# Kernel tuning notes

Measured on AMD Instinct MI355X. Metric: run time of the kernel, lower is better.

The kernel has to match this reference:

```python
import jax, jax.numpy as jnp
import numpy as np

SR = 16000
NYQ = SR / 2.0
N_FFT = 400
HOP = 160
WIN = 400
OUT_CHANNELS = 64
OUTPUT_SIZE = 64
MIN_LOW_HZ = 50.0
MIN_BAND_HZ = 50.0
FRAME_LENGTH = 400
EPS_LN = 1e-5


def _to_mel(hz):
    return 2595.0 * np.log10(1.0 + hz / 700.0)


def _to_hz(mel):
    return 700.0 * (10.0 ** (mel / 2595.0) - 1.0)


def setup_inputs() -> dict:
    key = jax.random.key(0)
    k1, = jax.random.split(key, 1)
    waveforms = jax.random.normal(k1, (1024, 1, 16000), dtype=jnp.float32)
    # mel-spaced init, exactly as in __init__ (freq_init='mel', range_constraint=False)
    low_hz = 30.0
    high_hz = NYQ - (MIN_LOW_HZ + MIN_BAND_HZ)
    mel = np.linspace(_to_mel(low_hz), _to_mel(high_hz), OUT_CHANNELS + 1)
    hz = _to_hz(mel)
    low_hz_ = jnp.asarray(hz[:-1], dtype=jnp.float32).reshape(-1, 1)
    band_hz_ = jnp.asarray(np.diff(hz), dtype=jnp.float32).reshape(-1, 1)
    ln_weight = jnp.ones((OUT_CHANNELS, 1), dtype=jnp.float32)
    ln_bias = jnp.zeros((OUT_CHANNELS, 1), dtype=jnp.float32)
    return {
        "waveforms": waveforms,
        "low_hz_": low_hz_,
        "band_hz_": band_hz_,
        "ln_weight": ln_weight,
        "ln_bias": ln_bias,
    }


def _hann_periodic(n):
    # torch.hann_window default: periodic=True
    k = jnp.arange(n, dtype=jnp.float32)
    return 0.5 - 0.5 * jnp.cos(2.0 * jnp.pi * k / n)


def _stft_mag(x):
    pad = N_FFT // 2
    xp = jnp.pad(x, ((0, 0), (pad, pad)), mode="reflect")
    n_frames = 1 + (xp.shape[1] - N_FFT) // HOP
    idx = jnp.arange(n_frames)[:, None] * HOP + jnp.arange(N_FFT)[None, :]
    frames = xp[:, idx] * _hann_periodic(WIN)  # [B, F_t, n_fft]
    spec = jnp.fft.rfft(frames, axis=-1)       # [B, F_t, n_fft//2+1]
    return jnp.abs(spec).transpose(0, 2, 1)    # [B, n_fft//2+1, F_t]


def _get_filters(low_hz_, band_hz_):
    # vectorized over all channels (original loops per channel)
    low = MIN_LOW_HZ + jnp.abs(low_hz_)                                   # [C,1]
    high = jnp.clip(low + MIN_BAND_HZ + jnp.abs(band_hz_), MIN_LOW_HZ, NYQ)
    freq = jnp.linspace(0.0, NYQ, N_FFT // 2 + 1, dtype=jnp.float32)      # [F]
    mask = (freq >= low) & (freq <= high)                                 # [C,F]
    center = (low + high) / 2.0
    bw = high - low
    resp = 1.0 - jnp.abs(freq - center) / (bw / 2.0)                      # triangular
    return jnp.where(mask, resp, 0.0)                                     # [C,F]


def _gln(x, weight, bias):
    # GlobalLayerNorm over dims (1,2) of [B,C,T]
    mean = jnp.mean(x, axis=(1, 2), keepdims=True)
    var = jnp.mean((x - mean) ** 2, axis=(1, 2), keepdims=True)
    return weight * (x - mean) / jnp.sqrt(var + EPS_LN) + bias


def _interp_linear(x, out_size):
    # torch F.interpolate(mode='linear', align_corners=False) along last dim
    t_in = x.shape[-1]
    scale = t_in / out_size
    pos = (jnp.arange(out_size, dtype=jnp.float32) + 0.5) * scale - 0.5
    pos = jnp.clip(pos, 0.0, t_in - 1)
    i0 = jnp.floor(pos).astype(jnp.int32)
    i1 = jnp.minimum(i0 + 1, t_in - 1)
    w = (pos - i0.astype(jnp.float32))
    return x[..., i0] * (1.0 - w) + x[..., i1] * w


def reference(waveforms, low_hz_, band_hz_, ln_weight, ln_bias):
    B = waveforms.shape[0]
    target_length = HOP * (OUTPUT_SIZE - 1) + FRAME_LENGTH  # 10480
    cur = waveforms.shape[-1]
    x = waveforms[:, 0, :]
    if target_length > cur:  # static shape decision
        x = jnp.pad(x, ((0, 0), (0, target_length - cur)))
    mag_spec = _stft_mag(x)                       # [B, 201, F_t]
    filters = _get_filters(low_hz_, band_hz_)     # [C, 201]
    filtered = jnp.einsum("cf,bft->bct", filters, mag_spec)  # [B, C, F_t]
    filtered = _gln(filtered, ln_weight, ln_bias)
    energy = filtered ** 2
    log_energy = jnp.log10(energy + 1e-6)         # [B, C, F_t]
    if log_energy.shape[-1] != OUTPUT_SIZE:
        log_energy = _interp_linear(log_energy, OUTPUT_SIZE)  # [B, C, 64]
    log_energy = log_energy[:, None, :, :].transpose(0, 1, 3, 2)  # [B,1,64,C]
    return (log_energy, filters)
```

## Files before the change

kernel.cpp:

```cpp
#include <hip/hip_runtime.h>
#include <math.h>

typedef __attribute__((ext_vector_type(8))) short short8;
typedef __attribute__((ext_vector_type(16))) float f32x16;
typedef __attribute__((ext_vector_type(8))) float f32x8;

__device__ inline unsigned short f2bf(float x) {
    unsigned u = __float_as_uint(x);
    unsigned r = u + 0x7fffu + ((u >> 16) & 1u);
    return (unsigned short)(r >> 16);
}

struct ASplit { short8 h, l; };

__device__ inline ASplit splitA(f32x8 v) {
    unsigned ah[4], al[4];
    #pragma unroll
    for (int q = 0; q < 4; ++q) {
        unsigned short h0 = f2bf(v[2*q]),   h1 = f2bf(v[2*q+1]);
        float hf0 = __uint_as_float((unsigned)h0 << 16);
        float hf1 = __uint_as_float((unsigned)h1 << 16);
        unsigned short l0 = f2bf(v[2*q] - hf0), l1 = f2bf(v[2*q+1] - hf1);
        ah[q] = (unsigned)h0 | ((unsigned)h1 << 16);
        al[q] = (unsigned)l0 | ((unsigned)l1 << 16);
    }
    ASplit r;
    r.h = __builtin_bit_cast(short8, *(uint4*)ah);
    r.l = __builtin_bit_cast(short8, *(uint4*)al);
    return r;
}

__device__ inline f32x8 loadA8(const float* __restrict__ x, int i0) {
    f32x8 r;
    if (i0 >= 0 && i0 <= 15992) {
        float4 a0 = *(const float4*)(x + i0);
        float4 a1 = *(const float4*)(x + i0 + 4);
        r[0] = a0.x; r[1] = a0.y; r[2] = a0.z; r[3] = a0.w;
        r[4] = a1.x; r[5] = a1.y; r[6] = a1.z; r[7] = a1.w;
    } else {
        #pragma unroll
        for (int e = 0; e < 8; ++e) {
            int p = i0 + e;
            p = (p < 0) ? -p : p;
            p = (p > 15999) ? (31998 - p) : p;
            r[e] = x[p];
        }
    }
    return r;
}

__device__ inline void filter_params(int c, const float* low_hz_, const float* band_hz_,
                                     float* fctr, float* finv, int* fks, int* fke) {
    float lo = 50.0f + fabsf(low_hz_[c]);
    float hi = lo + 50.0f + fabsf(band_hz_[c]);
    hi = fminf(fmaxf(hi, 50.0f), 8000.0f);
    float ctr = 0.5f * (lo + hi);
    float hbw = 0.5f * (hi - lo);
    int ks = (int)ceilf(lo * 0.025f);
    if (ks < 0) ks = 0;
    while (40.0f * (float)ks < lo) ++ks;
    while (ks > 0 && 40.0f * (float)(ks - 1) >= lo) --ks;
    int ke = (int)floorf(hi * 0.025f);
    if (ke > 200) ke = 200;
    while (40.0f * (float)ke > hi) --ke;
    while (ke < 200 && 40.0f * (float)(ke + 1) <= hi) ++ke;
    fctr[c] = ctr;
    finv[c] = (hbw > 0.0f) ? (1.0f / hbw) : 0.0f;
    fks[c]  = ks;
    fke[c]  = ke;
}

__global__ void fse_filters(const float* __restrict__ low_hz_,
                            const float* __restrict__ band_hz_,
                            float* __restrict__ out)
{
    int idx = blockIdx.x * 256 + threadIdx.x;
    if (idx >= 64 * 201) return;
    int c = idx / 201;
    int k = idx - c * 201;
    float lo = 50.0f + fabsf(low_hz_[c]);
    float hi = lo + 50.0f + fabsf(band_hz_[c]);
    hi = fminf(fmaxf(hi, 50.0f), 8000.0f);
    float ctr = 0.5f * (lo + hi);
    float hbw = 0.5f * (hi - lo);
    float fq = 40.0f * (float)k;
    float resp = 1.0f - fabsf(fq - ctr) / hbw;
    out[idx] = (fq >= lo && fq <= hi) ? resp : 0.0f;
}

__global__ void fse_setup_B(unsigned short* __restrict__ bt)
{
    int idx = blockIdx.x * 256 + threadIdx.x;
    if (idx >= 372736) return;
    int e   = idx & 7;
    int t   = idx >> 3;
    int row = t % 448;
    int q   = t / 448;
    int p   = q & 3;
    int pl  = (q >> 2) & 1;
    int kc  = q >> 3;
    int n   = kc * 32 + p * 8 + e;
    float v = 0.0f;
    if (n < 400) {
        int bin = -1, isim = 0;
        if (row <= 200) bin = row;
        else if (row >= 224 && row <= 424) { bin = row - 224; isim = 1; }
        if (bin >= 0) {
            int a = (bin * n) % 400;
            float th = 6.283185307179586f * ((float)a / 400.0f);
            float sn, cs;
            sincosf(th, &sn, &cs);
            float wn = 0.5f - 0.5f * cosf(6.283185307179586f * ((float)n / 400.0f));
            v = isim ? (-wn * sn) : (wn * cs);
        }
    }
    unsigned short h = f2bf(v);
    float hf = __uint_as_float((unsigned)h << 16);
    unsigned short l = f2bf(v - hf);
    bt[idx] = pl ? l : h;
}

__global__ __launch_bounds__(512, 4)
void fse_gemm(const float* __restrict__ wav,
              const float* __restrict__ low_hz_,
              const float* __restrict__ band_hz_,
              const unsigned short* __restrict__ Bt,
              float* __restrict__ filt)
{
    __shared__ __align__(16) char smem[57344];
    __shared__ float fctr[64], finv[64];
    __shared__ int   fks[64], fke[64];
    float* mags = (float*)smem;

    const int bid  = blockIdx.x;
    const int b    = bid >> 1;
    const int half = bid & 1;
    const int tid  = threadIdx.x;
    const int w    = tid >> 6;
    const int lane = tid & 63;
    const float* __restrict__ x = wav + b * 16000;

    if (tid < 64) filter_params(tid, low_hz_, band_hz_, fctr, finv, fks, fke);

    const int mt    = w >> 2;
    const int pq    = w & 3;
    const int pbase = pq * 2;
    const int cnt   = (pq < 3) ? 2 : 1;
    const int jrow  = lane & 31;
    const int g     = lane >> 5;

    const int arow = 64 * half + 32 * mt + jrow;
    const int te   = (arow <= 100) ? arow : 50;
    const int ab   = 160 * te - 200 + g * 8;

    f32x16 accR[2], accI[2];
    #pragma unroll
    for (int i = 0; i < 2; ++i)
        #pragma unroll
        for (int e = 0; e < 16; ++e) { accR[i][e] = 0.0f; accI[i][e] = 0.0f; }

    for (int kc = 0; kc < 13; ++kc) {
        __syncthreads();
        {
            const uint4* src = (const uint4*)Bt + kc * 3584 + (w << 6) + lane;
            char* dstb = smem + (w << 6) * 16;
            #pragma unroll
            for (int i = 0; i < 7; ++i) {
                __builtin_amdgcn_global_load_lds(
                    (const __attribute__((address_space(1))) unsigned*)(src + i * 512),
                    (__attribute__((address_space(3))) unsigned*)(dstb + i * 8192),
                    16, 0, 0);
            }
        }
        __syncthreads();

        f32x8 a0 = loadA8(x, ab + kc * 32);
        f32x8 a1 = loadA8(x, ab + kc * 32 + 16);

        const unsigned short* bs = (const unsigned short*)smem;
        #pragma unroll
        for (int s = 0; s < 2; ++s) {
            ASplit S = splitA(s ? a1 : a0);
            const int part = s * 2 + g;
            const int bhof = part * 3584;
            const int blof = (4 + part) * 3584;
            #pragma unroll
            for (int i = 0; i < 2; ++i) {
                if (i < cnt) {
                    const int p = pbase + i;
                    const int roR = p * 32 + jrow;
                    const int roI = (p + 7) * 32 + jrow;
                    short8 BhR = *(const short8*)(bs + bhof + roR * 8);
                    short8 BlR = *(const short8*)(bs + blof + roR * 8);
                    short8 BhI = *(const short8*)(bs + bhof + roI * 8);
                    short8 BlI = *(const short8*)(bs + blof + roI * 8);
                    accR[i] = __builtin_amdgcn_mfma_f32_32x32x16_bf16(S.h, BhR, accR[i], 0, 0, 0);
                    accR[i] = __builtin_amdgcn_mfma_f32_32x32x16_bf16(S.h, BlR, accR[i], 0, 0, 0);
                    accR[i] = __builtin_amdgcn_mfma_f32_32x32x16_bf16(S.l, BhR, accR[i], 0, 0, 0);
                    accI[i] = __builtin_amdgcn_mfma_f32_32x32x16_bf16(S.h, BhI, accI[i], 0, 0, 0);
                    accI[i] = __builtin_amdgcn_mfma_f32_32x32x16_bf16(S.h, BlI, accI[i], 0, 0, 0);
                    accI[i] = __builtin_amdgcn_mfma_f32_32x32x16_bf16(S.l, BhI, accI[i], 0, 0, 0);
                }
            }
        }
    }

    __syncthreads();

    #pragma unroll
    for (int i = 0; i < 2; ++i) {
        if (i < cnt) {
            const int k = (pbase + i) * 32 + jrow;
            if (k <= 200) {
                #pragma unroll
                for (int r = 0; r < 16; ++r) {
                    int tl = 32 * mt + (r & 3) + 8 * (r >> 2) + 4 * g;
                    float re = accR[i][r];
                    float im = accI[i][r];
                    mags[tl * 201 + k] = sqrtf(re * re + im * im);
                }
            }
        }
    }
    __syncthreads();

    const int tg = 64 * half + lane;
    #pragma unroll
    for (int i = 0; i < 8; ++i) {
        const int c = w * 8 + i;
        const float ctr = fctr[c];
        const float inv = finv[c];
        const int ks = fks[c], ke = fke[c];
        float a = 0.0f;
        for (int k = ks; k <= ke; ++k) {
            float resp = 1.0f - fabsf(40.0f * (float)k - ctr) * inv;
            a = fmaf(resp, mags[lane * 201 + k], a);
        }
        if (tg <= 100) filt[b * 6464 + c * 101 + tg] = a;
    }
}

__global__ __launch_bounds__(256)
void fse_post(const float* __restrict__ filt,
              const float* __restrict__ ln_w,
              const float* __restrict__ ln_b,
              float* __restrict__ out)
{
    __shared__ float fbuf[6464];
    __shared__ float red[8];
    __shared__ float stats[2];
    const int b    = blockIdx.x;
    const int tid  = threadIdx.x;
    const int w    = tid >> 6;
    const int lane = tid & 63;
    const float* __restrict__ src = filt + b * 6464;

    float s = 0.0f, ss = 0.0f;
    for (int i = tid; i < 6464; i += 256) {
        float v = src[i];
        fbuf[i] = v;
        s += v;
        ss = fmaf(v, v, ss);
    }
    #pragma unroll
    for (int off = 32; off > 0; off >>= 1) {
        s  += __shfl_down(s,  off, 64);
        ss += __shfl_down(ss, off, 64);
    }
    if (lane == 0) { red[w] = s; red[4 + w] = ss; }
    __syncthreads();
    if (tid == 0) {
        float ts = 0.0f, tss = 0.0f;
        for (int i = 0; i < 4; ++i) { ts += red[i]; tss += red[4 + i]; }
        float mu = ts * (1.0f / 6464.0f);
        stats[0] = mu;
        stats[1] = tss * (1.0f / 6464.0f) - mu * mu;
    }
    __syncthreads();
    const float mu   = stats[0];
    const float isig = 1.0f / sqrtf(stats[1] + 1e-5f);

    for (int idx = tid; idx < 4096; idx += 256) {
        const int to = idx >> 6;
        const int c  = idx & 63;
        float pos = ((float)to + 0.5f) * 1.578125f - 0.5f;
        pos = fminf(fmaxf(pos, 0.0f), 100.0f);
        int i0 = (int)floorf(pos);
        int i1 = i0 + 1; if (i1 > 100) i1 = 100;
        float fr = pos - (float)i0;
        float wc = ln_w[c], bc = ln_b[c];
        float x0 = fbuf[c * 101 + i0];
        float x1 = fbuf[c * 101 + i1];
        float y0 = fmaf(wc, (x0 - mu) * isig, bc);
        float y1 = fmaf(wc, (x1 - mu) * isig, bc);
        float l0 = log10f(fmaf(y0, y0, 1e-6f));
        float l1 = log10f(fmaf(y1, y1, 1e-6f));
        out[b * 4096 + idx] = l0 * (1.0f - fr) + l1 * fr;
    }
}

#define MSTR 209
__global__ __launch_bounds__(512, 2)
void fse_main_fused(const float* __restrict__ wav,
                    const float* __restrict__ low_hz_,
                    const float* __restrict__ band_hz_,
                    const float* __restrict__ ln_w,
                    const float* __restrict__ ln_b,
                    const unsigned short* __restrict__ Bt,
                    float* __restrict__ out)
{
    __shared__ __align__(16) char smem[114688];
    float* mags = (float*)smem;
    float* fbuf = (float*)(smem + 84544);
    __shared__ float fctr[64], finv[64];
    __shared__ int   fks[64], fke[64];
    __shared__ float red[16];
    __shared__ float stats[2];

    const int b    = blockIdx.x;
    const int tid  = threadIdx.x;
    const int w    = tid >> 6;
    const int lane = tid & 63;
    const float* __restrict__ x = wav + b * 16000;

    if (tid < 64) filter_params(tid, low_hz_, band_hz_, fctr, finv, fks, fke);

    const int mt   = w >> 1;
    const int half = w & 1;
    const int jrow = lane & 31;
    const int g    = lane >> 5;
    const int arow = mt * 32 + jrow;
    const int te   = (arow <= 100) ? arow : 50;
    const int abase = 160 * te - 200 + g * 8;

    const uint4* __restrict__ btg = (const uint4*)Bt;

    f32x8 ac0 = loadA8(x, abase);
    f32x8 ac1 = loadA8(x, abase + 16);
    {
        uint4 rr0 = btg[0 * 512 + tid], rr1 = btg[1 * 512 + tid];
        uint4 rr2 = btg[2 * 512 + tid], rr3 = btg[3 * 512 + tid];
        uint4 rr4 = btg[4 * 512 + tid], rr5 = btg[5 * 512 + tid];
        uint4 rr6 = btg[6 * 512 + tid];
        uint4* dst = (uint4*)smem;
        dst[0 * 512 + tid] = rr0; dst[1 * 512 + tid] = rr1;
        dst[2 * 512 + tid] = rr2; dst[3 * 512 + tid] = rr3;
        dst[4 * 512 + tid] = rr4; dst[5 * 512 + tid] = rr5;
        dst[6 * 512 + tid] = rr6;
    }
    __syncthreads();

    f32x16 acc[7];
    #pragma unroll
    for (int n = 0; n < 7; ++n)
        #pragma unroll
        for (int e = 0; e < 16; ++e) acc[n][e] = 0.0f;

    int curoff = 0;
    for (int kc = 0; kc < 13; ++kc) {
        const bool pre = (kc < 12);
        uint4 rr0, rr1, rr2, rr3, rr4, rr5, rr6;
        f32x8 an0, an1;
        if (pre) {
            const uint4* src = btg + (kc + 1) * 3584;
            rr0 = src[0 * 512 + tid]; rr1 = src[1 * 512 + tid];
            rr2 = src[2 * 512 + tid]; rr3 = src[3 * 512 + tid];
            rr4 = src[4 * 512 + tid]; rr5 = src[5 * 512 + tid];
            rr6 = src[6 * 512 + tid];
            an0 = loadA8(x, abase + (kc + 1) * 32);
            an1 = loadA8(x, abase + (kc + 1) * 32 + 16);
        }
        ASplit A0 = splitA(ac0);
        ASplit A1 = splitA(ac1);

        const unsigned short* bs = (const unsigned short*)(smem + curoff);
        #pragma unroll
        for (int s = 0; s < 2; ++s) {
            const short8 Ah = s ? A1.h : A0.h;
            const short8 Al = s ? A1.l : A0.l;
            const int pb = (s * 2 + g) * 448;
            #pragma unroll
            for (int n = 0; n < 7; ++n) {
                const int ro = (half * 7 + n) * 32 + jrow;
                short8 Bh = *(const short8*)(bs + (pb + ro) * 8);
                short8 Bl = *(const short8*)(bs + 14336 + (pb + ro) * 8);
                acc[n] = __builtin_amdgcn_mfma_f32_32x32x16_bf16(Ah, Bh, acc[n], 0, 0, 0);
                acc[n] = __builtin_amdgcn_mfma_f32_32x32x16_bf16(Ah, Bl, acc[n], 0, 0, 0);
                acc[n] = __builtin_amdgcn_mfma_f32_32x32x16_bf16(Al, Bh, acc[n], 0, 0, 0);
            }
        }
        if (pre) {
            uint4* dst = (uint4*)(smem + (curoff ^ 57344));
            dst[0 * 512 + tid] = rr0; dst[1 * 512 + tid] = rr1;
            dst[2 * 512 + tid] = rr2; dst[3 * 512 + tid] = rr3;
            dst[4 * 512 + tid] = rr4; dst[5 * 512 + tid] = rr5;
            dst[6 * 512 + tid] = rr6;
        }
        __syncthreads();
        if (pre) { ac0 = an0; ac1 = an1; }
        curoff ^= 57344;
    }

    if (half == 0) {
        #pragma unroll
        for (int n = 0; n < 7; ++n) {
            int k = n * 32 + jrow;
            if (k <= 200) {
                #pragma unroll
                for (int r = 0; r < 16; ++r) {
                    int t = mt * 32 + (r & 3) + 8 * (r >> 2) + 4 * g;
                    if (t <= 100) mags[t * MSTR + k] = acc[n][r];
                }
            }
        }
    }
    __syncthreads();
    if (half == 1) {
        #pragma unroll
        for (int n = 0; n < 7; ++n) {
            int k = n * 32 + jrow;
            if (k <= 200) {
                #pragma unroll
                for (int r = 0; r < 16; ++r) {
                    int t = mt * 32 + (r & 3) + 8 * (r >> 2) + 4 * g;
                    if (t <= 100) {
                        float re = mags[t * MSTR + k];
                        float im = acc[n][r];
                        mags[t * MSTR + k] = sqrtf(re * re + im * im);
                    }
                }
            }
        }
    }
    __syncthreads();

    {
        const int t0 = lane;
        const int t1v = 64 + lane;
        const int t1 = (t1v <= 100) ? t1v : 100;
        #pragma unroll
        for (int i = 0; i < 8; ++i) {
            const int c = w * 8 + i;
            const float ctr = fctr[c];
            const float inv = finv[c];
            const int ks = fks[c], ke = fke[c];
            float a0 = 0.0f, a1 = 0.0f;
            for (int k = ks; k <= ke; ++k) {
                float resp = 1.0f - fabsf(40.0f * (float)k - ctr) * inv;
                a0 = fmaf(resp, mags[t0 * MSTR + k], a0);
                a1 = fmaf(resp, mags[t1 * MSTR + k], a1);
            }
            fbuf[c * 101 + t0] = a0;
            if (t1v <= 100) fbuf[c * 101 + t1v] = a1;
        }
    }
    __syncthreads();

    float s = 0.0f, ss = 0.0f;
    for (int i = tid; i < 6464; i += 512) {
        float vv = fbuf[i];
        s += vv;
        ss = fmaf(vv, vv, ss);
    }
    #pragma unroll
    for (int off = 32; off > 0; off >>= 1) {
        s  += __shfl_down(s,  off, 64);
        ss += __shfl_down(ss, off, 64);
    }
    if (lane == 0) { red[w] = s; red[8 + w] = ss; }
    __syncthreads();
    if (tid == 0) {
        float ts = 0.0f, tss = 0.0f;
        for (int i = 0; i < 8; ++i) { ts += red[i]; tss += red[8 + i]; }
        float mu = ts * (1.0f / 6464.0f);
        stats[0] = mu;
        stats[1] = tss * (1.0f / 6464.0f) - mu * mu;
    }
    __syncthreads();
    const float mu   = stats[0];
    const float isig = 1.0f / sqrtf(stats[1] + 1e-5f);

    for (int idx = tid; idx < 4096; idx += 512) {
        const int to = idx >> 6;
        const int c  = idx & 63;
        float pos = ((float)to + 0.5f) * 1.578125f - 0.5f;
        pos = fminf(fmaxf(pos, 0.0f), 100.0f);
        int i0 = (int)floorf(pos);
        int i1 = i0 + 1; if (i1 > 100) i1 = 100;
        float fr = pos - (float)i0;
        float wc = ln_w[c], bc = ln_b[c];
        float x0 = fbuf[c * 101 + i0];
        float x1 = fbuf[c * 101 + i1];
        float y0 = fmaf(wc, (x0 - mu) * isig, bc);
        float y1 = fmaf(wc, (x1 - mu) * isig, bc);
        float l0 = log10f(fmaf(y0, y0, 1e-6f));
        float l1 = log10f(fmaf(y1, y1, 1e-6f));
        out[b * 4096 + idx] = l0 * (1.0f - fr) + l1 * fr;
    }
}

extern "C" void kernel_launch(void* const* d_in, const int* in_sizes, int n_in,
                              void* d_out, int out_size, void* d_ws, size_t ws_size,
                              hipStream_t stream)
{
    const float* wav = (const float*)d_in[0];
    const float* lo  = (const float*)d_in[1];
    const float* bd  = (const float*)d_in[2];
    const float* lw  = (const float*)d_in[3];
    const float* lb  = (const float*)d_in[4];
    float* out = (float*)d_out;

    fse_filters<<<(64 * 201 + 255) / 256, 256, 0, stream>>>(lo, bd, out + 1024 * 4096);

    const size_t BN1 = 745472;
    const size_t BN2 = BN1 + (size_t)1024 * 6464 * 4;
    unsigned short* Bts = (unsigned short*)d_ws;
    fse_setup_B<<<(372736 + 255) / 256, 256, 0, stream>>>(Bts);

    if (ws_size >= BN2) {
        float* filt = (float*)((char*)d_ws + BN1);
        fse_gemm<<<2048, 512, 0, stream>>>(wav, lo, bd, Bts, filt);
        fse_post<<<1024, 256, 0, stream>>>(filt, lw, lb, out);
    } else {
        fse_main_fused<<<1024, 512, 0, stream>>>(wav, lo, bd, lw, lb, Bts, out);
    }
}
```

Measured before the change: 249.7 us.

## Double-buffer B tiles in LDS with prefetch and cheaper bf16 split

Result: faster. 222.8 us (-10.8%).

```diff
diff --git a/kernel.cpp b/kernel.cpp
--- a/kernel.cpp
+++ b/kernel.cpp
@@ -27,6 +27,23 @@
     ASplit r;
     r.h = __builtin_bit_cast(short8, *(uint4*)ah);
     r.l = __builtin_bit_cast(short8, *(uint4*)al);
+    return r;
+}
+
+__device__ inline ASplit splitA_fast(f32x8 v) {
+    unsigned h[4], l[4];
+    #pragma unroll
+    for (int q = 0; q < 4; ++q) {
+        unsigned u0 = __float_as_uint(v[2*q]);
+        unsigned u1 = __float_as_uint(v[2*q+1]);
+        h[q] = __builtin_amdgcn_perm(u1, u0, 0x07060302u);
+        float r0 = v[2*q]   - __uint_as_float(u0 & 0xFFFF0000u);
+        float r1 = v[2*q+1] - __uint_as_float(u1 & 0xFFFF0000u);
+        l[q] = __builtin_amdgcn_perm(__float_as_uint(r1), __float_as_uint(r0), 0x07060302u);
+    }
+    ASplit r;
+    r.h = __builtin_bit_cast(short8, *(uint4*)h);
+    r.l = __builtin_bit_cast(short8, *(uint4*)l);
     return r;
 }
 
@@ -88,7 +105,39 @@
     out[idx] = (fq >= lo && fq <= hi) ? resp : 0.0f;
 }
 
-__global__ void fse_setup_B(unsigned short* __restrict__ bt)
+__global__ void fse_setup_B16(unsigned short* __restrict__ bt)
+{
+    int idx = blockIdx.x * 256 + threadIdx.x;
+    if (idx >= 372736) return;
+    int e   = idx & 7;
+    int t   = idx >> 3;
+    int row = t % 448;
+    int q   = t / 448;
+    int g   = q & 1;
+    int pl  = (q >> 1) & 1;
+    int kc  = q >> 2;
+    int n   = kc * 16 + g * 8 + e;
+    float v = 0.0f;
+    if (n < 400) {
+        int bin = -1, isim = 0;
+        if (row <= 200) bin = row;
+        else if (row >= 224 && row <= 424) { bin = row - 224; isim = 1; }
+        if (bin >= 0) {
+            int a = (bin * n) % 400;
+            float th = 6.283185307179586f * ((float)a / 400.0f);
+            float sn, cs;
+            sincosf(th, &sn, &cs);
+            float wn = 0.5f - 0.5f * cosf(6.283185307179586f * ((float)n / 400.0f));
+            v = isim ? (-wn * sn) : (wn * cs);
+        }
+    }
+    unsigned short h = f2bf(v);
+    float hf = __uint_as_float((unsigned)h << 16);
+    unsigned short l = f2bf(v - hf);
+    bt[idx] = pl ? l : h;
+}
+
+__global__ void fse_setup_B32(unsigned short* __restrict__ bt)
 {
     int idx = blockIdx.x * 256 + threadIdx.x;
     if (idx >= 372736) return;
@@ -153,59 +202,75 @@
     const int te   = (arow <= 100) ? arow : 50;
     const int ab   = 160 * te - 200 + g * 8;
 
+    const uint4* __restrict__ btg = (const uint4*)Bt;
+
+    f32x8 aC = loadA8(x, ab);
+    {
+        #pragma unroll
+        for (int i = 0; i < 4; ++i) {
+            int idx = i * 512 + tid;
+            if (idx < 1792) {
+                __builtin_amdgcn_global_load_lds(
+                    (const __attribute__((address_space(1))) unsigned*)(btg + idx),
+                    (__attribute__((address_space(3))) unsigned*)(smem + idx * 16),
+                    16, 0, 0);
+            }
+        }
+    }
+    __syncthreads();
+
     f32x16 accR[2], accI[2];
     #pragma unroll
     for (int i = 0; i < 2; ++i)
         #pragma unroll
         for (int e = 0; e < 16; ++e) { accR[i][e] = 0.0f; accI[i][e] = 0.0f; }
 
-    for (int kc = 0; kc < 13; ++kc) {
+    int cur = 0;
+    for (int kc = 0; kc < 26; ++kc) {
+        const bool pre = (kc < 25);
+        f32x8 aN;
+        if (pre) {
+            const uint4* src = btg + (kc + 1) * 1792;
+            const int bufo = cur ^ 28672;
+            #pragma unroll
+            for (int i = 0; i < 4; ++i) {
+                int idx = i * 512 + tid;
+                if (idx < 1792) {
+                    __builtin_amdgcn_global_load_lds(
+                        (const __attribute__((address_space(1))) unsigned*)(src + idx),
+                        (__attribute__((address_space(3))) unsigned*)(smem + bufo + idx * 16),
+                        16, 0, 0);
+                }
+            }
+            aN = loadA8(x, ab + (kc + 1) * 16);
+        }
+
+        ASplit S = splitA_fast(aC);
+
+        const unsigned short* bs = (const unsigned short*)(smem + cur);
+        #pragma unroll
+        for (int i = 0; i < 2; ++i) {
+            if (i < cnt) {
+                const int p = pbase + i;
+                const int roR = p * 32 + jrow;
+                const int roI = (p + 7) * 32 + jrow;
+                short8 BhR = *(const short8*)(bs + ((0 + g) * 448 + roR) * 8);
+                short8 BlR = *(const short8*)(bs + ((2 + g) * 448 + roR) * 8);
+                short8 BhI = *(const short8*)(bs + ((0 + g) * 448 + roI) * 8);
+                short8 BlI = *(const short8*)(bs + ((2 + g) * 448 + roI) * 8);
+                accR[i] = __builtin_amdgcn_mfma_f32_32x32x16_bf16(S.h, BhR, accR[i], 0, 0, 0);
+                accR[i] = __builtin_amdgcn_mfma_f32_32x32x16_bf16(S.h, BlR, accR[i], 0, 0, 0);
+                accR[i] = __builtin_amdgcn_mfma_f32_32x32x16_bf16(S.l, BhR, accR[i], 0, 0, 0);
+                accI[i] = __builtin_amdgcn_mfma_f32_32x32x16_bf16(S.h, BhI, accI[i], 0, 0, 0);
+                accI[i] = __builtin_amdgcn_mfma_f32_32x32x16_bf16(S.h, BlI, accI[i], 0, 0, 0);
+                accI[i] = __builtin_amdgcn_mfma_f32_32x32x16_bf16(S.l, BhI, accI[i], 0, 0, 0);
+            }
+        }
+
         __syncthreads();
-        {
-            const uint4* src = (const uint4*)Bt + kc * 3584 + (w << 6) + lane;
-            char* dstb = smem + (w << 6) * 16;
-            #pragma unroll
-            for (int i = 0; i < 7; ++i) {
-                __builtin_amdgcn_global_load_lds(
-                    (const __attribute__((address_space(1))) unsigned*)(src + i * 512),
-                    (__attribute__((address_space(3))) unsigned*)(dstb + i * 8192),
-                    16, 0, 0);
-            }
-        }
-        __syncthreads();
-
-        f32x8 a0 = loadA8(x, ab + kc * 32);
-        f32x8 a1 = loadA8(x, ab + kc * 32 + 16);
-
-        const unsigned short* bs = (const unsigned short*)smem;
-        #pragma unroll
-        for (int s = 0; s < 2; ++s) {
-            ASplit S = splitA(s ? a1 : a0);
-            const int part = s * 2 + g;
-            const int bhof = part * 3584;
-            const int blof = (4 + part) * 3584;
-            #pragma unroll
-            for (int i = 0; i < 2; ++i) {
-                if (i < cnt) {
-                    const int p = pbase + i;
-                    const int roR = p * 32 + jrow;
-                    const int roI = (p + 7) * 32 + jrow;
-                    short8 BhR = *(const short8*)(bs + bhof + roR * 8);
-                    short8 BlR = *(const short8*)(bs + blof + roR * 8);
-                    short8 BhI = *(const short8*)(bs + bhof + roI * 8);
-                    short8 BlI = *(const short8*)(bs + blof + roI * 8);
-                    accR[i] = __builtin_amdgcn_mfma_f32_32x32x16_bf16(S.h, BhR, accR[i], 0, 0, 0);
-                    accR[i] = __builtin_amdgcn_mfma_f32_32x32x16_bf16(S.h, BlR, accR[i], 0, 0, 0);
-                    accR[i] = __builtin_amdgcn_mfma_f32_32x32x16_bf16(S.l, BhR, accR[i], 0, 0, 0);
-                    accI[i] = __builtin_amdgcn_mfma_f32_32x32x16_bf16(S.h, BhI, accI[i], 0, 0, 0);
-                    accI[i] = __builtin_amdgcn_mfma_f32_32x32x16_bf16(S.h, BlI, accI[i], 0, 0, 0);
-                    accI[i] = __builtin_amdgcn_mfma_f32_32x32x16_bf16(S.l, BhI, accI[i], 0, 0, 0);
-                }
-            }
-        }
-    }
-
-    __syncthreads();
+        if (pre) aC = aN;
+        cur ^= 28672;
+    }
 
     #pragma unroll
     for (int i = 0; i < 2; ++i) {
@@ -515,13 +580,14 @@
     const size_t BN1 = 745472;
     const size_t BN2 = BN1 + (size_t)1024 * 6464 * 4;
     unsigned short* Bts = (unsigned short*)d_ws;
-    fse_setup_B<<<(372736 + 255) / 256, 256, 0, stream>>>(Bts);
 
     if (ws_size >= BN2) {
         float* filt = (float*)((char*)d_ws + BN1);
+        fse_setup_B16<<<(372736 + 255) / 256, 256, 0, stream>>>(Bts);
         fse_gemm<<<2048, 512, 0, stream>>>(wav, lo, bd, Bts, filt);
         fse_post<<<1024, 256, 0, stream>>>(filt, lw, lb, out);
     } else {
+        fse_setup_B32<<<(372736 + 255) / 256, 256, 0, stream>>>(Bts);
         fse_main_fused<<<1024, 512, 0, stream>>>(wav, lo, bd, lw, lb, Bts, out);
     }
 }
```

## Fuse GEMM and post-processing into one 1024-thread kernel with double-buffered LDS

Applied to the files above, without the earlier changes.

After: 219.5 us. -12.1%, faster.

```diff
diff --git a/kernel.cpp b/kernel.cpp
--- a/kernel.cpp
+++ b/kernel.cpp
@@ -1,5 +1,8 @@
 #include <hip/hip_runtime.h>
 #include <math.h>
+
+#define BLOCK 1024
+#define MSTR 209
 
 typedef __attribute__((ext_vector_type(8))) short short8;
 typedef __attribute__((ext_vector_type(16))) float f32x16;
@@ -13,20 +16,20 @@
 
 struct ASplit { short8 h, l; };
 
-__device__ inline ASplit splitA(f32x8 v) {
-    unsigned ah[4], al[4];
+__device__ inline ASplit splitA_fast(f32x8 v) {
+    unsigned h[4], l[4];
     #pragma unroll
     for (int q = 0; q < 4; ++q) {
-        unsigned short h0 = f2bf(v[2*q]),   h1 = f2bf(v[2*q+1]);
-        float hf0 = __uint_as_float((unsigned)h0 << 16);
-        float hf1 = __uint_as_float((unsigned)h1 << 16);
-        unsigned short l0 = f2bf(v[2*q] - hf0), l1 = f2bf(v[2*q+1] - hf1);
-        ah[q] = (unsigned)h0 | ((unsigned)h1 << 16);
-        al[q] = (unsigned)l0 | ((unsigned)l1 << 16);
+        unsigned u0 = __float_as_uint(v[2*q]);
+        unsigned u1 = __float_as_uint(v[2*q+1]);
+        h[q] = __builtin_amdgcn_perm(u1, u0, 0x07060302u);
+        float r0 = v[2*q]   - __uint_as_float(u0 & 0xFFFF0000u);
+        float r1 = v[2*q+1] - __uint_as_float(u1 & 0xFFFF0000u);
+        l[q] = __builtin_amdgcn_perm(__float_as_uint(r1), __float_as_uint(r0), 0x07060302u);
     }
     ASplit r;
-    r.h = __builtin_bit_cast(short8, *(uint4*)ah);
-    r.l = __builtin_bit_cast(short8, *(uint4*)al);
+    r.h = __builtin_bit_cast(short8, *(uint4*)h);
+    r.l = __builtin_bit_cast(short8, *(uint4*)l);
     return r;
 }
 
@@ -120,21 +123,25 @@
     bt[idx] = pl ? l : h;
 }
 
-__global__ __launch_bounds__(512, 4)
-void fse_gemm(const float* __restrict__ wav,
+__global__ __launch_bounds__(1024, 4)
+void fse_main(const float* __restrict__ wav,
               const float* __restrict__ low_hz_,
               const float* __restrict__ band_hz_,
+              const float* __restrict__ ln_w,
+              const float* __restrict__ ln_b,
               const unsigned short* __restrict__ Bt,
-              float* __restrict__ filt)
+              float* __restrict__ out)
 {
-    __shared__ __align__(16) char smem[57344];
+    __shared__ __align__(16) char smem[114688];
+    float* mags = (float*)smem;
+    float* fbuf = (float*)(smem + 84544);
+
     __shared__ float fctr[64], finv[64];
     __shared__ int   fks[64], fke[64];
-    float* mags = (float*)smem;
-
-    const int bid  = blockIdx.x;
-    const int b    = bid >> 1;
-    const int half = bid & 1;
+    __shared__ float red[32];
+    __shared__ float stats[2];
+
+    const int b    = blockIdx.x;
     const int tid  = threadIdx.x;
     const int w    = tid >> 6;
     const int lane = tid & 63;
@@ -149,9 +156,27 @@
     const int jrow  = lane & 31;
     const int g     = lane >> 5;
 
-    const int arow = 64 * half + 32 * mt + jrow;
+    const int arow = 32 * mt + jrow;
     const int te   = (arow <= 100) ? arow : 50;
     const int ab   = 160 * te - 200 + g * 8;
+
+    const uint4* __restrict__ btg = (const uint4*)Bt;
+
+    f32x8 aC0 = loadA8(x, ab);
+    f32x8 aC1 = loadA8(x, ab + 16);
+    {
+        #pragma unroll
+        for (int i = 0; i < 4; ++i) {
+            int idx = i * 1024 + tid;
+            if (idx < 3584) {
+                __builtin_amdgcn_global_load_lds(
+                    (const __attribute__((address_space(1))) unsigned*)(btg + idx),
+                    (__attribute__((address_space(3))) unsigned*)(smem + idx * 16),
+                    16, 0, 0);
+            }
+        }
+    }
+    __syncthreads();
 
     f32x16 accR[2], accI[2];
     #pragma unroll
@@ -159,28 +184,35 @@
         #pragma unroll
         for (int e = 0; e < 16; ++e) { accR[i][e] = 0.0f; accI[i][e] = 0.0f; }
 
+    int cur = 0;
     for (int kc = 0; kc < 13; ++kc) {
-        __syncthreads();
-        {
-            const uint4* src = (const uint4*)Bt + kc * 3584 + (w << 6) + lane;
-            char* dstb = smem + (w << 6) * 16;
+        const bool pre = (kc < 12);
+
+        ASplit S0 = splitA_fast(aC0);
+        ASplit S1 = splitA_fast(aC1);
+
+        if (pre) {
+            const uint4* src = btg + (kc + 1) * 3584;
+            const int bufo = cur ^ 57344;
             #pragma unroll
-            for (int i = 0; i < 7; ++i) {
-                __builtin_amdgcn_global_load_lds(
-                    (const __attribute__((address_space(1))) unsigned*)(src + i * 512),
-                    (__attribute__((address_space(3))) unsigned*)(dstb + i * 8192),
-                    16, 0, 0);
-            }
-        }
-        __syncthreads();
-
-        f32x8 a0 = loadA8(x, ab + kc * 32);
-        f32x8 a1 = loadA8(x, ab + kc * 32 + 16);
-
-        const unsigned short* bs = (const unsigned short*)smem;
+            for (int i = 0; i < 4; ++i) {
+                int idx = i * 1024 + tid;
+                if (idx < 3584) {
+                    __builtin_amdgcn_global_load_lds(
+                        (const __attribute__((address_space(1))) unsigned*)(src + idx),
+                        (__attribute__((address_space(3))) unsigned*)(smem + bufo + idx * 16),
+                        16, 0, 0);
+                }
+            }
+            aC0 = loadA8(x, ab + (kc + 1) * 32);
+            aC1 = loadA8(x, ab + (kc + 1) * 32 + 16);
+        }
+
+        const unsigned short* bs = (const unsigned short*)(smem + cur);
         #pragma unroll
         for (int s = 0; s < 2; ++s) {
-            ASplit S = splitA(s ? a1 : a0);
+            const short8 Ah = s ? S1.h : S0.h;
+            const short8 Al = s ? S1.l : S0.l;
             const int part = s * 2 + g;
             const int bhof = part * 3584;
             const int blof = (4 + part) * 3584;
@@ -194,18 +226,19 @@
                     short8 BlR = *(const short8*)(bs + blof + roR * 8);
                     short8 BhI = *(const short8*)(bs + bhof + roI * 8);
                     short8 BlI = *(const short8*)(bs + blof + roI * 8);
-                    accR[i] = __builtin_amdgcn_mfma_f32_32x32x16_bf16(S.h, BhR, accR[i], 0, 0, 0);
-                    accR[i] = __builtin_amdgcn_mfma_f32_32x32x16_bf16(S.h, BlR, accR[i], 0, 0, 0);
-                    accR[i] = __builtin_amdgcn_mfma_f32_32x32x16_bf16(S.l, BhR, accR[i], 0, 0, 0);
-                    accI[i] = __builtin_amdgcn_mfma_f32_32x32x16_bf16(S.h, BhI, accI[i], 0, 0, 0);
-                    accI[i] = __builtin_amdgcn_mfma_f32_32x32x16_bf16(S.h, BlI, accI[i], 0, 0, 0);
-                    accI[i] = __builtin_amdgcn_mfma_f32_32x32x16_bf16(S.l, BhI, accI[i], 0, 0, 0);
+                    accR[i] = __builtin_amdgcn_mfma_f32_32x32x16_bf16(Ah, BhR, accR[i], 0, 0, 0);
+                    accR[i] = __builtin_amdgcn_mfma_f32_32x32x16_bf16(Ah, BlR, accR[i], 0, 0, 0);
+                    accR[i] = __builtin_amdgcn_mfma_f32_32x32x16_bf16(Al, BhR, accR[i], 0, 0, 0);
+                    accI[i] = __builtin_amdgcn_mfma_f32_32x32x16_bf16(Ah, BhI, accI[i], 0, 0, 0);
+                    accI[i] = __builtin_amdgcn_mfma_f32_32x32x16_bf16(Ah, BlI, accI[i], 0, 0, 0);
+                    accI[i] = __builtin_amdgcn_mfma_f32_32x32x16_bf16(Al, BhI, accI[i], 0, 0, 0);
                 }
             }
         }
-    }
-
-    __syncthreads();
+
+        __syncthreads();
+        cur ^= 57344;
+    }
 
     #pragma unroll
     for (int i = 0; i < 2; ++i) {
@@ -214,64 +247,56 @@
             if (k <= 200) {
                 #pragma unroll
                 for (int r = 0; r < 16; ++r) {
-                    int tl = 32 * mt + (r & 3) + 8 * (r >> 2) + 4 * g;
-                    float re = accR[i][r];
-                    float im = accI[i][r];
-                    mags[tl * 201 + k] = sqrtf(re * re + im * im);
+                    int t = 32 * mt + (r & 3) + 8 * (r >> 2) + 4 * g;
+                    if (t <= 100) {
+                        float re = accR[i][r];
+                        float im = accI[i][r];
+                        mags[t * MSTR + k] = sqrtf(re * re + im * im);
+                    }
                 }
             }
         }
     }
     __syncthreads();
 
-    const int tg = 64 * half + lane;
-    #pragma unroll
-    for (int i = 0; i < 8; ++i) {
-        const int c = w * 8 + i;
-        const float ctr = fctr[c];
-        const float inv = finv[c];
-        const int ks = fks[c], ke = fke[c];
-        float a = 0.0f;
-        for (int k = ks; k <= ke; ++k) {
-            float resp = 1.0f - fabsf(40.0f * (float)k - ctr) * inv;
-            a = fmaf(resp, mags[lane * 201 + k], a);
-        }
-        if (tg <= 100) filt[b * 6464 + c * 101 + tg] = a;
-    }
-}
-
-__global__ __launch_bounds__(256)
-void fse_post(const float* __restrict__ filt,
-              const float* __restrict__ ln_w,
-              const float* __restrict__ ln_b,
-              float* __restrict__ out)
-{
-    __shared__ float fbuf[6464];
-    __shared__ float red[8];
-    __shared__ float stats[2];
-    const int b    = blockIdx.x;
-    const int tid  = threadIdx.x;
-    const int w    = tid >> 6;
-    const int lane = tid & 63;
-    const float* __restrict__ src = filt + b * 6464;
+    {
+        const int t0 = lane;
+        const int t1v = 64 + lane;
+        const int t1 = (t1v <= 100) ? t1v : 100;
+        #pragma unroll
+        for (int i = 0; i < 4; ++i) {
+            const int c = w * 4 + i;
+            const float ctr = fctr[c];
+            const float inv = finv[c];
+            const int ks = fks[c], ke = fke[c];
+            float a0 = 0.0f, a1 = 0.0f;
+            for (int k = ks; k <= ke; ++k) {
+                float resp = 1.0f - fabsf(40.0f * (float)k - ctr) * inv;
+                a0 = fmaf(resp, mags[t0 * MSTR + k], a0);
+                a1 = fmaf(resp, mags[t1 * MSTR + k], a1);
+            }
+            fbuf[c * 101 + t0] = a0;
+            if (t1v <= 100) fbuf[c * 101 + t1v] = a1;
+        }
+    }
+    __syncthreads();
 
     float s = 0.0f, ss = 0.0f;
-    for (int i = tid; i < 6464; i += 256) {
-        float v = src[i];
-        fbuf[i] = v;
-        s += v;
-        ss = fmaf(v, v, ss);
+    for (int i = tid; i < 6464; i += BLOCK) {
+        float vv = fbuf[i];
+        s += vv;
+        ss = fmaf(vv, vv, ss);
     }
     #pragma unroll
     for (int off = 32; off > 0; off >>= 1) {
         s  += __shfl_down(s,  off, 64);
         ss += __shfl_down(ss, off, 64);
     }
-    if (lane == 0) { red[w] = s; red[4 + w] = ss; }
+    if (lane == 0) { red[w] = s; red[16 + w] = ss; }
     __syncthreads();
     if (tid == 0) {
         float ts = 0.0f, tss = 0.0f;
-        for (int i = 0; i < 4; ++i) { ts += red[i]; tss += red[4 + i]; }
+        for (int i = 0; i < 16; ++i) { ts += red[i]; tss += red[16 + i]; }
         float mu = ts * (1.0f / 6464.0f);
         stats[0] = mu;
         stats[1] = tss * (1.0f / 6464.0f) - mu * mu;
@@ -280,7 +305,7 @@
     const float mu   = stats[0];
     const float isig = 1.0f / sqrtf(stats[1] + 1e-5f);
 
-    for (int idx = tid; idx < 4096; idx += 256) {
+    for (int idx = tid; idx < 4096; idx += BLOCK) {
         const int to = idx >> 6;
         const int c  = idx & 63;
         float pos = ((float)to + 0.5f) * 1.578125f - 0.5f;
@@ -299,206 +324,6 @@
     }
 }
 
-#define MSTR 209
-__global__ __launch_bounds__(512, 2)
-void fse_main_fused(const float* __restrict__ wav,
-                    const float* __restrict__ low_hz_,
-                    const float* __restrict__ band_hz_,
-                    const float* __restrict__ ln_w,
-                    const float* __restrict__ ln_b,
-                    const unsigned short* __restrict__ Bt,
-                    float* __restrict__ out)
-{
-    __shared__ __align__(16) char smem[114688];
-    float* mags = (float*)smem;
-    float* fbuf = (float*)(smem + 84544);
-    __shared__ float fctr[64], finv[64];
-    __shared__ int   fks[64], fke[64];
-    __shared__ float red[16];
-    __shared__ float stats[2];
-
-    const int b    = blockIdx.x;
-    const int tid  = threadIdx.x;
-    const int w    = tid >> 6;
-    const int lane = tid & 63;
-    const float* __restrict__ x = wav + b * 16000;
-
-    if (tid < 64) filter_params(tid, low_hz_, band_hz_, fctr, finv, fks, fke);
-
-    const int mt   = w >> 1;
-    const int half = w & 1;
-    const int jrow = lane & 31;
-    const int g    = lane >> 5;
-    const int arow = mt * 32 + jrow;
-    const int te   = (arow <= 100) ? arow : 50;
-    const int abase = 160 * te - 200 + g * 8;
-
-    const uint4* __restrict__ btg = (const uint4*)Bt;
-
-    f32x8 ac0 = loadA8(x, abase);
-    f32x8 ac1 = loadA8(x, abase + 16);
-    {
-        uint4 rr0 = btg[0 * 512 + tid], rr1 = btg[1 * 512 + tid];
-        uint4 rr2 = btg[2 * 512 + tid], rr3 = btg[3 * 512 + tid];
-        uint4 rr4 = btg[4 * 512 + tid], rr5 = btg[5 * 512 + tid];
-        uint4 rr6 = btg[6 * 512 + tid];
-        uint4* dst = (uint4*)smem;
-        dst[0 * 512 + tid] = rr0; dst[1 * 512 + tid] = rr1;
-        dst[2 * 512 + tid] = rr2; dst[3 * 512 + tid] = rr3;
-        dst[4 * 512 + tid] = rr4; dst[5 * 512 + tid] = rr5;
-        dst[6 * 512 + tid] = rr6;
-    }
-    __syncthreads();
-
-    f32x16 acc[7];
-    #pragma unroll
-    for (int n = 0; n < 7; ++n)
-        #pragma unroll
-        for (int e = 0; e < 16; ++e) acc[n][e] = 0.0f;
-
-    int curoff = 0;
-    for (int kc = 0; kc < 13; ++kc) {
-        const bool pre = (kc < 12);
-        uint4 rr0, rr1, rr2, rr3, rr4, rr5, rr6;
-        f32x8 an0, an1;
-        if (pre) {
-            const uint4* src = btg + (kc + 1) * 3584;
-            rr0 = src[0 * 512 + tid]; rr1 = src[1 * 512 + tid];
-            rr2 = src[2 * 512 + tid]; rr3 = src[3 * 512 + tid];
-            rr4 = src[4 * 512 + tid]; rr5 = src[5 * 512 + tid];
-            rr6 = src[6 * 512 + tid];
-            an0 = loadA8(x, abase + (kc + 1) * 32);
-            an1 = loadA8(x, abase + (kc + 1) * 32 + 16);
-        }
-        ASplit A0 = splitA(ac0);
-        ASplit A1 = splitA(ac1);
-
-        const unsigned short* bs = (const unsigned short*)(smem + curoff);
-        #pragma unroll
-        for (int s = 0; s < 2; ++s) {
-            const short8 Ah = s ? A1.h : A0.h;
-            const short8 Al = s ? A1.l : A0.l;
-            const int pb = (s * 2 + g) * 448;
-            #pragma unroll
-            for (int n = 0; n < 7; ++n) {
-                const int ro = (half * 7 + n) * 32 + jrow;
-                short8 Bh = *(const short8*)(bs + (pb + ro) * 8);
-                short8 Bl = *(const short8*)(bs + 14336 + (pb + ro) * 8);
-                acc[n] = __builtin_amdgcn_mfma_f32_32x32x16_bf16(Ah, Bh, acc[n], 0, 0, 0);
-                acc[n] = __builtin_amdgcn_mfma_f32_32x32x16_bf16(Ah, Bl, acc[n], 0, 0, 0);
-                acc[n] = __builtin_amdgcn_mfma_f32_32x32x16_bf16(Al, Bh, acc[n], 0, 0, 0);
-            }
-        }
-        if (pre) {
-            uint4* dst = (uint4*)(smem + (curoff ^ 57344));
-            dst[0 * 512 + tid] = rr0; dst[1 * 512 + tid] = rr1;
-            dst[2 * 512 + tid] = rr2; dst[3 * 512 + tid] = rr3;
-            dst[4 * 512 + tid] = rr4; dst[5 * 512 + tid] = rr5;
-            dst[6 * 512 + tid] = rr6;
-        }
-        __syncthreads();
-        if (pre) { ac0 = an0; ac1 = an1; }
-        curoff ^= 57344;
-    }
-
-    if (half == 0) {
-        #pragma unroll
-        for (int n = 0; n < 7; ++n) {
-            int k = n * 32 + jrow;
-            if (k <= 200) {
-                #pragma unroll
-                for (int r = 0; r < 16; ++r) {
-                    int t = mt * 32 + (r & 3) + 8 * (r >> 2) + 4 * g;
-                    if (t <= 100) mags[t * MSTR + k] = acc[n][r];
-                }
-            }
-        }
-    }
-    __syncthreads();
-    if (half == 1) {
-        #pragma unroll
-        for (int n = 0; n < 7; ++n) {
-            int k = n * 32 + jrow;
-            if (k <= 200) {
-                #pragma unroll
-                for (int r = 0; r < 16; ++r) {
-                    int t = mt * 32 + (r & 3) + 8 * (r >> 2) + 4 * g;
-                    if (t <= 100) {
-                        float re = mags[t * MSTR + k];
-                        float im = acc[n][r];
-                        mags[t * MSTR + k] = sqrtf(re * re + im * im);
-                    }
-                }
-            }
-        }
-    }
-    __syncthreads();
-
-    {
-        const int t0 = lane;
-        const int t1v = 64 + lane;
-        const int t1 = (t1v <= 100) ? t1v : 100;
-        #pragma unroll
-        for (int i = 0; i < 8; ++i) {
-            const int c = w * 8 + i;
-            const float ctr = fctr[c];
-            const float inv = finv[c];
-            const int ks = fks[c], ke = fke[c];
-            float a0 = 0.0f, a1 = 0.0f;
-            for (int k = ks; k <= ke; ++k) {
-                float resp = 1.0f - fabsf(40.0f * (float)k - ctr) * inv;
-                a0 = fmaf(resp, mags[t0 * MSTR + k], a0);
-                a1 = fmaf(resp, mags[t1 * MSTR + k], a1);
-            }
-            fbuf[c * 101 + t0] = a0;
-            if (t1v <= 100) fbuf[c * 101 + t1v] = a1;
-        }
-    }
-    __syncthreads();
-
-    float s = 0.0f, ss = 0.0f;
-    for (int i = tid; i < 6464; i += 512) {
-        float vv = fbuf[i];
-        s += vv;
-        ss = fmaf(vv, vv, ss);
-    }
-    #pragma unroll
-    for (int off = 32; off > 0; off >>= 1) {
-        s  += __shfl_down(s,  off, 64);
-        ss += __shfl_down(ss, off, 64);
-    }
-    if (lane == 0) { red[w] = s; red[8 + w] = ss; }
-    __syncthreads();
-    if (tid == 0) {
-        float ts = 0.0f, tss = 0.0f;
-        for (int i = 0; i < 8; ++i) { ts += red[i]; tss += red[8 + i]; }
-        float mu = ts * (1.0f / 6464.0f);
-        stats[0] = mu;
-        stats[1] = tss * (1.0f / 6464.0f) - mu * mu;
-    }
-    __syncthreads();
-    const float mu   = stats[0];
-    const float isig = 1.0f / sqrtf(stats[1] + 1e-5f);
-
-    for (int idx = tid; idx < 4096; idx += 512) {
-        const int to = idx >> 6;
-        const int c  = idx & 63;
-        float pos = ((float)to + 0.5f) * 1.578125f - 0.5f;
-        pos = fminf(fmaxf(pos, 0.0f), 100.0f);
-        int i0 = (int)floorf(pos);
-        int i1 = i0 + 1; if (i1 > 100) i1 = 100;
-        float fr = pos - (float)i0;
-        float wc = ln_w[c], bc = ln_b[c];
-        float x0 = fbuf[c * 101 + i0];
-        float x1 = fbuf[c * 101 + i1];
-        float y0 = fmaf(wc, (x0 - mu) * isig, bc);
-        float y1 = fmaf(wc, (x1 - mu) * isig, bc);
-        float l0 = log10f(fmaf(y0, y0, 1e-6f));
-        float l1 = log10f(fmaf(y1, y1, 1e-6f));
-        out[b * 4096 + idx] = l0 * (1.0f - fr) + l1 * fr;
-    }
-}
-
 extern "C" void kernel_launch(void* const* d_in, const int* in_sizes, int n_in,
                               void* d_out, int out_size, void* d_ws, size_t ws_size,
                               hipStream_t stream)
@@ -512,16 +337,7 @@
 
     fse_filters<<<(64 * 201 + 255) / 256, 256, 0, stream>>>(lo, bd, out + 1024 * 4096);
 
-    const size_t BN1 = 745472;
-    const size_t BN2 = BN1 + (size_t)1024 * 6464 * 4;
     unsigned short* Bts = (unsigned short*)d_ws;
     fse_setup_B<<<(372736 + 255) / 256, 256, 0, stream>>>(Bts);
-
-    if (ws_size >= BN2) {
-        float* filt = (float*)((char*)d_ws + BN1);
-        fse_gemm<<<2048, 512, 0, stream>>>(wav, lo, bd, Bts, filt);
-        fse_post<<<1024, 256, 0, stream>>>(filt, lw, lb, out);
-    } else {
-        fse_main_fused<<<1024, 512, 0, stream>>>(wav, lo, bd, lw, lb, Bts, out);
-    }
-}
+    fse_main<<<1024, BLOCK, 0, stream>>>(wav, lo, bd, lw, lb, Bts, out);
+}
```
